# Kernel tuning notes

Hardware: AMD Instinct MI355X
Metric: run time of the kernel (lower is better)

The kernel has to match this reference:

```python
import jax, jax.numpy as jnp
import numpy as np

NEG_SLOPE = 0.2  # PyG GATConv default negative_slope


def gat_conv(x, W, b, a_src, a_dst, src, dst, N, H, C):
    """PyG-style GATConv (v1 attention), concat heads, self-loops already in (src,dst)."""
    h = (x @ W).reshape(N, H, C)                       # [N,H,C]
    al_src = jnp.sum(h * a_src, axis=-1)               # [N,H]
    al_dst = jnp.sum(h * a_dst, axis=-1)               # [N,H]
    e = jax.nn.leaky_relu(al_src[src] + al_dst[dst], NEG_SLOPE)  # [E,H]
    m = jax.ops.segment_max(e, dst, num_segments=N)    # segment softmax (stable)
    m = jnp.where(jnp.isfinite(m), m, 0.0)
    ex = jnp.exp(e - m[dst])
    denom = jax.ops.segment_sum(ex, dst, num_segments=N)
    alpha = ex / (denom[dst] + 1e-16)                  # [E,H]
    msg = h[src] * alpha[..., None]                    # [E,H,C]
    out = jax.ops.segment_sum(msg, dst, num_segments=N)  # [N,H,C]
    return out.reshape(N, H * C) + b


def setup_inputs() -> dict:
    key = jax.random.key(0)
    ks = jax.random.split(key, 16)
    N, E, IN, HID, HEADS, OUT, G = 50000, 600000, 128, 64, 4, 10, 64
    x = jax.random.normal(ks[0], (N, IN), dtype=jnp.float32)
    edge_index = jax.random.randint(ks[1], (2, E), 0, N, dtype=jnp.int32)
    batch = jnp.sort(jax.random.randint(ks[2], (N,), 0, G, dtype=jnp.int32))
    s = 0.1
    p = {
        'W1': jax.random.normal(ks[3], (IN, HEADS * HID)) * s,
        'b1': jnp.zeros((HEADS * HID,), jnp.float32),
        'asrc1': jax.random.normal(ks[4], (HEADS, HID)) * s,
        'adst1': jax.random.normal(ks[5], (HEADS, HID)) * s,
        'W2': jax.random.normal(ks[6], (HEADS * HID, HEADS * HID)) * s,
        'b2': jnp.zeros((HEADS * HID,), jnp.float32),
        'asrc2': jax.random.normal(ks[7], (HEADS, HID)) * s,
        'adst2': jax.random.normal(ks[8], (HEADS, HID)) * s,
        'W3': jax.random.normal(ks[9], (HEADS * HID, HID)) * s,
        'b3': jnp.zeros((HID,), jnp.float32),
        'asrc3': jax.random.normal(ks[10], (1, HID)) * s,
        'adst3': jax.random.normal(ks[11], (1, HID)) * s,
        'linW': jax.random.normal(ks[12], (HID, OUT)) * s,
        'linb': jnp.zeros((OUT,), jnp.float32),
    }
    return dict(x=x, edge_index=edge_index, batch=batch, **p)


def reference(x, edge_index, batch, W1, b1, asrc1, adst1, W2, b2, asrc2, adst2,
              W3, b3, asrc3, adst3, linW, linb):
    N = x.shape[0]
    G = 64  # number of graphs
    loops = jnp.arange(N, dtype=edge_index.dtype)
    src = jnp.concatenate([edge_index[0], loops])  # PyG adds self-loops by default
    dst = jnp.concatenate([edge_index[1], loops])
    # eval mode: dropout is identity
    h = jax.nn.elu(gat_conv(x, W1, b1, asrc1, adst1, src, dst, N, 4, 64))
    h = jax.nn.elu(gat_conv(h, W2, b2, asrc2, adst2, src, dst, N, 4, 64))
    h = jax.nn.elu(gat_conv(h, W3, b3, asrc3, adst3, src, dst, N, 1, 64))
    # global mean pool over graphs
    sums = jax.ops.segment_sum(h, batch, num_segments=G)            # [G,64]
    cnts = jax.ops.segment_sum(jnp.ones((N,), h.dtype), batch, num_segments=G)
    pooled = sums / jnp.maximum(cnts, 1.0)[:, None]
    return pooled @ linW + linb                                      # [G,10]
```

## Files before the change

kernel.cpp:

```cpp
#include <hip/hip_runtime.h>
#include <hip/hip_bf16.h>
#include <math.h>

#define NEG_SLOPE 0.2f

typedef short short8 __attribute__((ext_vector_type(8)));
typedef float f32x4 __attribute__((ext_vector_type(4)));
typedef unsigned int u32;
typedef unsigned short u16;

__device__ __forceinline__ float lrelu(float x){ return x > 0.f ? x : NEG_SLOPE * x; }
__device__ __forceinline__ float elu_f(float x){ return x > 0.f ? x : __expf(x) - 1.f; }
__device__ __forceinline__ float blo(u32 w){ return __uint_as_float(w << 16); }
__device__ __forceinline__ float bhi(u32 w){ return __uint_as_float(w & 0xffff0000u); }
__device__ __forceinline__ float bf2f(u16 u){ return __uint_as_float(((u32)u) << 16); }
__device__ __forceinline__ u16 f2bf(float f){
  __hip_bfloat16 h = __float2bfloat16(f);
  return *(u16*)&h;
}

__global__ void prep_kernel(const float* __restrict__ x, u16* __restrict__ xb, int n4,
                            const float* __restrict__ W1, u16* __restrict__ w1t,
                            const float* __restrict__ W2, u16* __restrict__ w2t,
                            const float* __restrict__ W3, u16* __restrict__ w3t,
                            int* __restrict__ cursor, int N){
  int i = blockIdx.x * 256 + threadIdx.x;
  if (i < n4){
    float4 v = ((const float4*)x)[i];
    ushort4 o;
    o.x = f2bf(v.x); o.y = f2bf(v.y); o.z = f2bf(v.z); o.w = f2bf(v.w);
    ((ushort4*)xb)[i] = o;
    return;
  }
  int t = i - n4;
  if (t < 128 * 256){
    int k = t >> 8, m = t & 255;
    w1t[m * 128 + k] = f2bf(W1[t]);
    return;
  }
  t -= 128 * 256;
  if (t < 256 * 256){
    int k = t >> 8, m = t & 255;
    w2t[m * 256 + k] = f2bf(W2[t]);
    return;
  }
  t -= 256 * 256;
  if (t < 256 * 64){
    int k = t >> 6, m = t & 63;
    w3t[m * 256 + k] = f2bf(W3[t]);
    return;
  }
  t -= 256 * 64;
  if (t < N) cursor[t] = 0;
}

__global__ void ell_kernel(const int* __restrict__ src, const int* __restrict__ dst,
                           int E, int* cursor, int* __restrict__ ell){
  int i = blockIdx.x * 256 + threadIdx.x;
  if (i < E){
    int s = src[i], d = dst[i];
    int pos = atomicAdd(&cursor[d], 1);
    if (pos < 64) ell[(size_t)d * 64 + pos] = s;
  }
}

template<int BN>
__global__ __launch_bounds__((BN == 256) ? 512 : 256) void gemm_mfma(
    const u16* __restrict__ A, const u16* __restrict__ Bt, u16* __restrict__ C,
    const float* __restrict__ asrc, const float* __restrict__ adst,
    float* __restrict__ als, float* __restrict__ ald, int N, int K, int M){
  constexpr int T  = (BN == 256) ? 512 : 256;
  constexpr int MI = (BN == 256) ? 4 : 2;
  constexpr int HH = BN / 64;
  constexpr int AQ = 1024 / T;
  constexpr int SB = BN * 8 / T;
  constexpr int LB = (BN == 256) ? 8 : 6;
  __shared__ short As[8][128][8];
  __shared__ short Bs[8][BN][8];
  const int tid = threadIdx.x;
  const int w = tid >> 6, lane = tid & 63;
  const int quad = lane >> 4, l16 = lane & 15;
  const int row0 = blockIdx.y * 128;
  const int wrow = (BN == 256) ? (w >> 2) * 64 : w * 32;
  const int wcol = (BN == 256) ? (w & 3) * 64 : 0;

  f32x4 acc[MI][4];
#pragma unroll
  for (int i = 0; i < MI; i++)
#pragma unroll
    for (int j = 0; j < 4; j++) acc[i][j] = (f32x4){0.f, 0.f, 0.f, 0.f};

  for (int k0 = 0; k0 < K; k0 += 64){
    __syncthreads();
#pragma unroll
    for (int q = 0; q < AQ; q++){
      int lb = q * T + w * 64;
      int li = lb + lane;
      int c = li >> 7, r = li & 127;
      int grow = min(row0 + r, N - 1);
      const u16* gp = A + (size_t)grow * K + k0 + c * 8;
      __builtin_amdgcn_global_load_lds((const __attribute__((address_space(1))) void*)gp,
                                       (__attribute__((address_space(3))) void*)((char*)&As[0][0][0] + (size_t)lb * 16),
                                       16, 0, 0);
    }
#pragma unroll
    for (int q = 0; q < SB; q++){
      int lb = q * T + w * 64;
      int li = lb + lane;
      int c = li >> LB, n = li & (BN - 1);
      const u16* gp = Bt + (size_t)n * K + k0 + c * 8;
      __builtin_amdgcn_global_load_lds((const __attribute__((address_space(1))) void*)gp,
                                       (__attribute__((address_space(3))) void*)((char*)&Bs[0][0][0] + (size_t)lb * 16),
                                       16, 0, 0);
    }
    __syncthreads();
#pragma unroll
    for (int ks = 0; ks < 2; ks++){
      short8 a[MI], b[4];
#pragma unroll
      for (int i = 0; i < MI; i++) a[i] = *(const short8*)&As[ks * 4 + quad][wrow + i * 16 + l16][0];
#pragma unroll
      for (int j = 0; j < 4; j++)  b[j] = *(const short8*)&Bs[ks * 4 + quad][wcol + j * 16 + l16][0];
#pragma unroll
      for (int i = 0; i < MI; i++)
#pragma unroll
        for (int j = 0; j < 4; j++)
          acc[i][j] = __builtin_amdgcn_mfma_f32_16x16x32_bf16(a[i], b[j], acc[i][j], 0, 0, 0);
    }
  }

  const int head = wcol >> 6;
  float avs[4], avd[4];
#pragma unroll
  for (int j = 0; j < 4; j++){
    int c = j * 16 + l16;
    avs[j] = asrc[head * 64 + c];
    avd[j] = adst[head * 64 + c];
  }

#pragma unroll
  for (int i = 0; i < MI; i++){
#pragma unroll
    for (int rr = 0; rr < 4; rr++){
      int row = row0 + wrow + i * 16 + quad * 4 + rr;
      float ps = acc[i][0][rr] * avs[0] + acc[i][1][rr] * avs[1]
               + acc[i][2][rr] * avs[2] + acc[i][3][rr] * avs[3];
      float pd = acc[i][0][rr] * avd[0] + acc[i][1][rr] * avd[1]
               + acc[i][2][rr] * avd[2] + acc[i][3][rr] * avd[3];
#pragma unroll
      for (int off = 8; off > 0; off >>= 1){
        ps += __shfl_xor(ps, off);
        pd += __shfl_xor(pd, off);
      }
      if (row < N){
#pragma unroll
        for (int j = 0; j < 4; j++)
          C[(size_t)row * M + wcol + j * 16 + l16] = f2bf(acc[i][j][rr]);
        if (l16 == 0){
          als[(size_t)row * HH + head] = ps;
          ald[(size_t)row * HH + head] = pd;
        }
      }
    }
  }
}

__global__ __launch_bounds__(256) void agg4_kernel(const u16* __restrict__ hb,
    const float* __restrict__ als, const float* __restrict__ ald,
    const int* __restrict__ degv, const int* __restrict__ ell,
    const float* __restrict__ bias, u16* __restrict__ out, int N){
  __shared__ float lex[4][256];
  __shared__ int lu[4][64];
  int wslot = threadIdx.x >> 6;
  int node = (blockIdx.x * 256 + threadIdx.x) >> 6;
  int lane = threadIdx.x & 63;
  if (node >= N) return;
  int deg = min(degv[node], 64);
  float4 t4 = *(const float4*)(ald + node * 4);
  const int hh = lane >> 4;

  bool v = lane < deg;
  int u = v ? ell[(size_t)node * 64 + lane] : 0;
  float4 s = *(const float4*)(als + (size_t)u * 4);
  float4 exv;
  exv.x = v ? __expf(lrelu(s.x + t4.x)) : 0.f;
  exv.y = v ? __expf(lrelu(s.y + t4.y)) : 0.f;
  exv.z = v ? __expf(lrelu(s.z + t4.z)) : 0.f;
  exv.w = v ? __expf(lrelu(s.w + t4.w)) : 0.f;
  *(float4*)&lex[wslot][lane * 4] = exv;
  lu[wslot][lane] = u;
  asm volatile("s_waitcnt lgkmcnt(0)" ::: "memory");

  const u16* hbl = hb + lane * 4;
  float4 ss = *(const float4*)(als + (size_t)node * 4);
  float es0 = __expf(lrelu(ss.x + t4.x));
  float es1 = __expf(lrelu(ss.y + t4.y));
  float es2 = __expf(lrelu(ss.z + t4.z));
  float es3 = __expf(lrelu(ss.w + t4.w));
  float exs = (hh == 0) ? es0 : (hh == 1) ? es1 : (hh == 2) ? es2 : es3;
  uint2 tself = *(const uint2*)(hbl + (size_t)node * 256);
  float denom = exs;
  float a0 = exs * blo(tself.x), a1 = exs * bhi(tself.x);
  float a2 = exs * blo(tself.y), a3 = exs * bhi(tself.y);

#pragma unroll 8
  for (int jj = 0; jj < deg; jj++){
    float ex = lex[wslot][jj * 4 + hh];
    int uu = lu[wslot][jj];
    uint2 t = *(const uint2*)(hbl + (size_t)uu * 256);
    denom += ex;
    a0 += ex * blo(t.x);
    a1 += ex * bhi(t.x);
    a2 += ex * blo(t.y);
    a3 += ex * bhi(t.y);
  }
  float inv = 1.f / (denom + 1e-16f);
  int ch = lane * 4;
  float o0 = elu_f(a0 * inv + bias[ch]);
  float o1 = elu_f(a1 * inv + bias[ch + 1]);
  float o2 = elu_f(a2 * inv + bias[ch + 2]);
  float o3 = elu_f(a3 * inv + bias[ch + 3]);
  uint2 o;
  o.x = (u32)f2bf(o0) | ((u32)f2bf(o1) << 16);
  o.y = (u32)f2bf(o2) | ((u32)f2bf(o3) << 16);
  ((uint2*)out)[(size_t)node * 64 + lane] = o;
}

__global__ __launch_bounds__(256) void agg1_kernel(const u16* __restrict__ hb,
    const float* __restrict__ als, const float* __restrict__ ald,
    const int* __restrict__ degv, const int* __restrict__ ell,
    const float* __restrict__ bias, u16* __restrict__ out, int N){
  __shared__ float lex[4][72];
  __shared__ int lu[4][72];
  int wslot = threadIdx.x >> 6;
  int node = (blockIdx.x * 256 + threadIdx.x) >> 6;
  int lane = threadIdx.x & 63;
  if (node >= N) return;
  int deg = min(degv[node], 64);
  float adv = ald[node];

  bool v = lane < deg;
  int u = v ? ell[(size_t)node * 64 + lane] : 0;
  lex[wslot][lane] = v ? __expf(lrelu(als[u] + adv)) : 0.f;
  lu[wslot][lane] = u;
  if (lane < 8){ lex[wslot][64 + lane] = 0.f; lu[wslot][64 + lane] = 0; }
  asm volatile("s_waitcnt lgkmcnt(0)" ::: "memory");

  int eo = lane >> 4;
  int chb = (lane & 15) * 4;
  float a0 = 0.f, a1 = 0.f, a2 = 0.f, a3 = 0.f, denom = 0.f;
  if (eo == 0){
    float exs = __expf(lrelu(als[node] + adv));
    uint2 t = *(const uint2*)(hb + (size_t)node * 64 + chb);
    denom = exs;
    a0 = exs * blo(t.x); a1 = exs * bhi(t.x);
    a2 = exs * blo(t.y); a3 = exs * bhi(t.y);
  }
#pragma unroll 4
  for (int j2 = 0; j2 < deg; j2 += 4){
    int jj = j2 + eo;
    float ex = lex[wslot][jj];
    int uu = lu[wslot][jj];
    uint2 t = *(const uint2*)(hb + (size_t)uu * 64 + chb);
    denom += ex;
    a0 += ex * blo(t.x);
    a1 += ex * bhi(t.x);
    a2 += ex * blo(t.y);
    a3 += ex * bhi(t.y);
  }
#pragma unroll
  for (int off = 16; off < 64; off <<= 1){
    denom += __shfl_xor(denom, off);
    a0 += __shfl_xor(a0, off); a1 += __shfl_xor(a1, off);
    a2 += __shfl_xor(a2, off); a3 += __shfl_xor(a3, off);
  }
  if (eo == 0){
    float inv = 1.f / (denom + 1e-16f);
    float o0 = elu_f(a0 * inv + bias[chb]);
    float o1 = elu_f(a1 * inv + bias[chb + 1]);
    float o2 = elu_f(a2 * inv + bias[chb + 2]);
    float o3 = elu_f(a3 * inv + bias[chb + 3]);
    uint2 o;
    o.x = (u32)f2bf(o0) | ((u32)f2bf(o1) << 16);
    o.y = (u32)f2bf(o2) | ((u32)f2bf(o3) << 16);
    *(uint2*)(out + (size_t)node * 64 + chb) = o;
  }
}

__global__ __launch_bounds__(256) void poolfinal_kernel(const u16* __restrict__ f,
    const int* __restrict__ batch, int N, const float* __restrict__ linW,
    const float* __restrict__ linb, float* __restrict__ out){
  const int g = blockIdx.x;
  const int w = threadIdx.x >> 6, lane = threadIdx.x & 63;
  int lo = 0, hi = N;
  while (lo < hi){ int m = (lo + hi) >> 1; if (batch[m] < g) lo = m + 1; else hi = m; }
  const int s0 = lo;
  lo = 0; hi = N;
  while (lo < hi){ int m = (lo + hi) >> 1; if (batch[m] < g + 1) lo = m + 1; else hi = m; }
  const int s1 = lo;

  float acc0 = 0.f, acc1 = 0.f, acc2 = 0.f, acc3 = 0.f;
  int n = s0 + w;
  for (; n + 12 < s1; n += 16){
    acc0 += bf2f(f[(size_t)n * 64 + lane]);
    acc1 += bf2f(f[(size_t)(n + 4) * 64 + lane]);
    acc2 += bf2f(f[(size_t)(n + 8) * 64 + lane]);
    acc3 += bf2f(f[(size_t)(n + 12) * 64 + lane]);
  }
  for (; n < s1; n += 4) acc0 += bf2f(f[(size_t)n * 64 + lane]);
  float acc = (acc0 + acc1) + (acc2 + acc3);

  __shared__ float red[4][64];
  red[w][lane] = acc;
  __syncthreads();
  if (threadIdx.x < 64){
    red[0][lane] = red[0][lane] + red[1][lane] + red[2][lane] + red[3][lane];
  }
  __syncthreads();
  if (threadIdx.x < 10){
    float c = fmaxf((float)(s1 - s0), 1.f);
    float a = 0.f;
#pragma unroll
    for (int k = 0; k < 64; k++) a += red[0][k] * linW[k * 10 + threadIdx.x];
    out[g * 10 + threadIdx.x] = a / c + linb[threadIdx.x];
  }
}

extern "C" void kernel_launch(void* const* d_in, const int* in_sizes, int n_in,
                              void* d_out, int out_size, void* d_ws, size_t ws_size,
                              hipStream_t stream) {
  const float* x     = (const float*)d_in[0];
  const int*   ei    = (const int*)  d_in[1];
  const int*   batch = (const int*)  d_in[2];
  const float* W1    = (const float*)d_in[3];
  const float* b1    = (const float*)d_in[4];
  const float* asrc1 = (const float*)d_in[5];
  const float* adst1 = (const float*)d_in[6];
  const float* W2    = (const float*)d_in[7];
  const float* b2    = (const float*)d_in[8];
  const float* asrc2 = (const float*)d_in[9];
  const float* adst2 = (const float*)d_in[10];
  const float* W3    = (const float*)d_in[11];
  const float* b3    = (const float*)d_in[12];
  const float* asrc3 = (const float*)d_in[13];
  const float* adst3 = (const float*)d_in[14];
  const float* linW  = (const float*)d_in[15];
  const float* linb  = (const float*)d_in[16];

  const int N = in_sizes[0] / 128;
  const int E = in_sizes[1] / 2;
  const int G = 64;
  const int* src = ei;
  const int* dst = ei + E;

  char* p = (char*)d_ws;
  auto carve = [&](size_t bytes) -> char* {
    char* r = p;
    p += (bytes + 255) & ~(size_t)255;
    return r;
  };
  u16*   xb       = (u16*)  carve((size_t)N * 128 * 2);
  u16*   w1t      = (u16*)  carve((size_t)256 * 128 * 2);
  u16*   w2t      = (u16*)  carve((size_t)256 * 256 * 2);
  u16*   w3t      = (u16*)  carve((size_t)64 * 256 * 2);
  u16*   hb       = (u16*)  carve((size_t)N * 256 * 2);
  u16*   featb    = (u16*)  carve((size_t)N * 256 * 2);
  u16*   out3     = (u16*)  carve((size_t)N * 64 * 2);
  float* als      = (float*)carve((size_t)N * 4 * 4);
  float* ald      = (float*)carve((size_t)N * 4 * 4);
  int*   cursor   = (int*)  carve((size_t)N * 4);
  int*   ell      = (int*)  carve((size_t)N * 64 * 4);

  const int n4 = N * 128 / 4;
  const int prep_items = n4 + 128 * 256 + 256 * 256 + 256 * 64 + N;

  prep_kernel<<<(prep_items + 255) / 256, 256, 0, stream>>>(x, xb, n4, W1, w1t, W2, w2t, W3, w3t,
                                                            cursor, N);

  ell_kernel<<<(E + 255) / 256, 256, 0, stream>>>(src, dst, E, cursor, ell);

  const int nby = (N + 127) / 128;
  const int wpn_grid = (N + 3) / 4;

  gemm_mfma<256><<<dim3(1, nby), 512, 0, stream>>>(xb, w1t, hb, asrc1, adst1, als, ald, N, 128, 256);
  agg4_kernel<<<wpn_grid, 256, 0, stream>>>(hb, als, ald, cursor, ell, b1, featb, N);

  gemm_mfma<256><<<dim3(1, nby), 512, 0, stream>>>(featb, w2t, hb, asrc2, adst2, als, ald, N, 256, 256);
  agg4_kernel<<<wpn_grid, 256, 0, stream>>>(hb, als, ald, cursor, ell, b2, featb, N);

  gemm_mfma<64><<<dim3(1, nby), 256, 0, stream>>>(featb, w3t, hb, asrc3, adst3, als, ald, N, 256, 64);
  agg1_kernel<<<wpn_grid, 256, 0, stream>>>(hb, als, ald, cursor, ell, b3, out3, N);

  poolfinal_kernel<<<G, 256, 0, stream>>>(out3, batch, N, linW, linb, (float*)d_out);
}
```

Measured before the change: 341.2 us.

## Fuse GAT aggregation into following layer's MFMA GEMM via LDS A-tile

Replaces the standalone 4-head aggregation kernels with a fused kernel. Each block aggregates 128 destination nodes directly into a swizzled LDS A tile, then runs the next layer's bf16 MFMA GEMM and attention-logit epilogue on that tile. This removes the write and re-read of the intermediate bf16 feature matrix and one launch per layer. Attention logits are ping-ponged between two buffers so the fused kernel never reads and writes the same array. The cost is far fewer blocks (one per 128 nodes) doing serial per-node gathers, which may expose gather latency and lower occupancy because of the large LDS footprint.

Measured after the change: 476.9 us. +39.8%, slower.

```diff
diff --git a/kernel.cpp b/kernel.cpp
--- a/kernel.cpp
+++ b/kernel.cpp
@@ -165,65 +165,163 @@
   }
 }
 
-__global__ __launch_bounds__(256) void agg4_kernel(const u16* __restrict__ hb,
-    const float* __restrict__ als, const float* __restrict__ ald,
+template<int BN>
+__global__ __launch_bounds__((BN == 256) ? 512 : 256) void fused_agg_gemm(
+    const u16* __restrict__ Gsrc,
+    const float* __restrict__ als_in, const float* __restrict__ ald_in,
     const int* __restrict__ degv, const int* __restrict__ ell,
-    const float* __restrict__ bias, u16* __restrict__ out, int N){
-  __shared__ float lex[4][256];
-  __shared__ int lu[4][64];
-  int wslot = threadIdx.x >> 6;
-  int node = (blockIdx.x * 256 + threadIdx.x) >> 6;
-  int lane = threadIdx.x & 63;
-  if (node >= N) return;
-  int deg = min(degv[node], 64);
-  float4 t4 = *(const float4*)(ald + node * 4);
+    const float* __restrict__ bias_in,
+    const u16* __restrict__ Bt, u16* __restrict__ C,
+    const float* __restrict__ asrc, const float* __restrict__ adst,
+    float* __restrict__ als_out, float* __restrict__ ald_out, int N){
+  constexpr int K   = 256;
+  constexpr int T   = (BN == 256) ? 512 : 256;
+  constexpr int W   = T / 64;
+  constexpr int NPW = 128 / W;
+  constexpr int MI  = (BN == 256) ? 4 : 2;
+  constexpr int HH  = BN / 64;
+  constexpr int SB  = BN * 8 / T;
+  constexpr int LB  = (BN == 256) ? 8 : 6;
+  __shared__ short As[128][32][8];
+  __shared__ short Bs[8][BN][8];
+  __shared__ float lexs[W][256];
+  __shared__ int   lus[W][64];
+  const int tid = threadIdx.x;
+  const int w = tid >> 6, lane = tid & 63;
+  const int quad = lane >> 4, l16 = lane & 15;
+  const int row0 = blockIdx.x * 128;
+  const int wrow = (BN == 256) ? (w >> 2) * 64 : w * 32;
+  const int wcol = (BN == 256) ? (w & 3) * 64 : 0;
   const int hh = lane >> 4;
 
-  bool v = lane < deg;
-  int u = v ? ell[(size_t)node * 64 + lane] : 0;
-  float4 s = *(const float4*)(als + (size_t)u * 4);
-  float4 exv;
-  exv.x = v ? __expf(lrelu(s.x + t4.x)) : 0.f;
-  exv.y = v ? __expf(lrelu(s.y + t4.y)) : 0.f;
-  exv.z = v ? __expf(lrelu(s.z + t4.z)) : 0.f;
-  exv.w = v ? __expf(lrelu(s.w + t4.w)) : 0.f;
-  *(float4*)&lex[wslot][lane * 4] = exv;
-  lu[wslot][lane] = u;
-  asm volatile("s_waitcnt lgkmcnt(0)" ::: "memory");
-
-  const u16* hbl = hb + lane * 4;
-  float4 ss = *(const float4*)(als + (size_t)node * 4);
-  float es0 = __expf(lrelu(ss.x + t4.x));
-  float es1 = __expf(lrelu(ss.y + t4.y));
-  float es2 = __expf(lrelu(ss.z + t4.z));
-  float es3 = __expf(lrelu(ss.w + t4.w));
-  float exs = (hh == 0) ? es0 : (hh == 1) ? es1 : (hh == 2) ? es2 : es3;
-  uint2 tself = *(const uint2*)(hbl + (size_t)node * 256);
-  float denom = exs;
-  float a0 = exs * blo(tself.x), a1 = exs * bhi(tself.x);
-  float a2 = exs * blo(tself.y), a3 = exs * bhi(tself.y);
-
+  for (int nn = 0; nn < NPW; nn++){
+    int r = w * NPW + nn;
+    int node = row0 + r;
+    float o0 = 0.f, o1 = 0.f, o2 = 0.f, o3 = 0.f;
+    if (node < N){
+      int deg = min(degv[node], 64);
+      float4 t4 = *(const float4*)(ald_in + (size_t)node * 4);
+      bool v = lane < deg;
+      int u = v ? ell[(size_t)node * 64 + lane] : 0;
+      float4 s = *(const float4*)(als_in + (size_t)u * 4);
+      float4 exv;
+      exv.x = v ? __expf(lrelu(s.x + t4.x)) : 0.f;
+      exv.y = v ? __expf(lrelu(s.y + t4.y)) : 0.f;
+      exv.z = v ? __expf(lrelu(s.z + t4.z)) : 0.f;
+      exv.w = v ? __expf(lrelu(s.w + t4.w)) : 0.f;
+      *(float4*)&lexs[w][lane * 4] = exv;
+      lus[w][lane] = u;
+      asm volatile("s_waitcnt lgkmcnt(0)" ::: "memory");
+
+      const u16* gl = Gsrc + lane * 4;
+      float4 ss = *(const float4*)(als_in + (size_t)node * 4);
+      float es0 = __expf(lrelu(ss.x + t4.x));
+      float es1 = __expf(lrelu(ss.y + t4.y));
+      float es2 = __expf(lrelu(ss.z + t4.z));
+      float es3 = __expf(lrelu(ss.w + t4.w));
+      float exs = (hh == 0) ? es0 : (hh == 1) ? es1 : (hh == 2) ? es2 : es3;
+      uint2 tself = *(const uint2*)(gl + (size_t)node * 256);
+      float denom = exs;
+      float a0 = exs * blo(tself.x), a1 = exs * bhi(tself.x);
+      float a2 = exs * blo(tself.y), a3 = exs * bhi(tself.y);
 #pragma unroll 8
-  for (int jj = 0; jj < deg; jj++){
-    float ex = lex[wslot][jj * 4 + hh];
-    int uu = lu[wslot][jj];
-    uint2 t = *(const uint2*)(hbl + (size_t)uu * 256);
-    denom += ex;
-    a0 += ex * blo(t.x);
-    a1 += ex * bhi(t.x);
-    a2 += ex * blo(t.y);
-    a3 += ex * bhi(t.y);
-  }
-  float inv = 1.f / (denom + 1e-16f);
-  int ch = lane * 4;
-  float o0 = elu_f(a0 * inv + bias[ch]);
-  float o1 = elu_f(a1 * inv + bias[ch + 1]);
-  float o2 = elu_f(a2 * inv + bias[ch + 2]);
-  float o3 = elu_f(a3 * inv + bias[ch + 3]);
-  uint2 o;
-  o.x = (u32)f2bf(o0) | ((u32)f2bf(o1) << 16);
-  o.y = (u32)f2bf(o2) | ((u32)f2bf(o3) << 16);
-  ((uint2*)out)[(size_t)node * 64 + lane] = o;
+      for (int jj = 0; jj < deg; jj++){
+        float ex = lexs[w][jj * 4 + hh];
+        int uu = lus[w][jj];
+        uint2 t = *(const uint2*)(gl + (size_t)uu * 256);
+        denom += ex;
+        a0 += ex * blo(t.x);
+        a1 += ex * bhi(t.x);
+        a2 += ex * blo(t.y);
+        a3 += ex * bhi(t.y);
+      }
+      float inv = 1.f / (denom + 1e-16f);
+      int ch = lane * 4;
+      o0 = elu_f(a0 * inv + bias_in[ch]);
+      o1 = elu_f(a1 * inv + bias_in[ch + 1]);
+      o2 = elu_f(a2 * inv + bias_in[ch + 2]);
+      o3 = elu_f(a3 * inv + bias_in[ch + 3]);
+    }
+    uint2 pk;
+    pk.x = (u32)f2bf(o0) | ((u32)f2bf(o1) << 16);
+    pk.y = (u32)f2bf(o2) | ((u32)f2bf(o3) << 16);
+    int bo = (r * 512 + lane * 8) ^ ((r & 7) << 4);
+    *(uint2*)((char*)&As[0][0][0] + bo) = pk;
+  }
+
+  f32x4 acc[MI][4];
+#pragma unroll
+  for (int i = 0; i < MI; i++)
+#pragma unroll
+    for (int j = 0; j < 4; j++) acc[i][j] = (f32x4){0.f, 0.f, 0.f, 0.f};
+
+  for (int t = 0; t < 4; t++){
+    __syncthreads();
+#pragma unroll
+    for (int q = 0; q < SB; q++){
+      int lb = q * T + w * 64;
+      int li = lb + lane;
+      int c = li >> LB, n = li & (BN - 1);
+      const u16* gp = Bt + (size_t)n * K + t * 64 + c * 8;
+      __builtin_amdgcn_global_load_lds((const __attribute__((address_space(1))) void*)gp,
+                                       (__attribute__((address_space(3))) void*)((char*)&Bs[0][0][0] + (size_t)lb * 16),
+                                       16, 0, 0);
+    }
+    __syncthreads();
+#pragma unroll
+    for (int ks = 0; ks < 2; ks++){
+      int kg = t * 8 + ks * 4 + quad;
+      short8 a[MI], b[4];
+#pragma unroll
+      for (int i = 0; i < MI; i++){
+        int row = wrow + i * 16 + l16;
+        int bo = (row * 512 + kg * 16) ^ ((row & 7) << 4);
+        a[i] = *(const short8*)((const char*)&As[0][0][0] + bo);
+      }
+#pragma unroll
+      for (int j = 0; j < 4; j++) b[j] = *(const short8*)&Bs[ks * 4 + quad][wcol + j * 16 + l16][0];
+#pragma unroll
+      for (int i = 0; i < MI; i++)
+#pragma unroll
+        for (int j = 0; j < 4; j++)
+          acc[i][j] = __builtin_amdgcn_mfma_f32_16x16x32_bf16(a[i], b[j], acc[i][j], 0, 0, 0);
+    }
+  }
+
+  const int head = wcol >> 6;
+  float avs[4], avd[4];
+#pragma unroll
+  for (int j = 0; j < 4; j++){
+    int c = j * 16 + l16;
+    avs[j] = asrc[head * 64 + c];
+    avd[j] = adst[head * 64 + c];
+  }
+
+#pragma unroll
+  for (int i = 0; i < MI; i++){
+#pragma unroll
+    for (int rr = 0; rr < 4; rr++){
+      int row = row0 + wrow + i * 16 + quad * 4 + rr;
+      float ps = acc[i][0][rr] * avs[0] + acc[i][1][rr] * avs[1]
+               + acc[i][2][rr] * avs[2] + acc[i][3][rr] * avs[3];
+      float pd = acc[i][0][rr] * avd[0] + acc[i][1][rr] * avd[1]
+               + acc[i][2][rr] * avd[2] + acc[i][3][rr] * avd[3];
+#pragma unroll
+      for (int off = 8; off > 0; off >>= 1){
+        ps += __shfl_xor(ps, off);
+        pd += __shfl_xor(pd, off);
+      }
+      if (row < N){
+#pragma unroll
+        for (int j = 0; j < 4; j++)
+          C[(size_t)row * BN + wcol + j * 16 + l16] = f2bf(acc[i][j][rr]);
+        if (l16 == 0){
+          als_out[(size_t)row * HH + head] = ps;
+          ald_out[(size_t)row * HH + head] = pd;
+        }
+      }
+    }
+  }
 }
 
 __global__ __launch_bounds__(256) void agg1_kernel(const u16* __restrict__ hb,
@@ -366,8 +464,10 @@
   u16*   hb       = (u16*)  carve((size_t)N * 256 * 2);
   u16*   featb    = (u16*)  carve((size_t)N * 256 * 2);
   u16*   out3     = (u16*)  carve((size_t)N * 64 * 2);
-  float* als      = (float*)carve((size_t)N * 4 * 4);
-  float* ald      = (float*)carve((size_t)N * 4 * 4);
+  float* alsA     = (float*)carve((size_t)N * 4 * 4);
+  float* aldA     = (float*)carve((size_t)N * 4 * 4);
+  float* alsB     = (float*)carve((size_t)N * 4 * 4);
+  float* aldB     = (float*)carve((size_t)N * 4 * 4);
   int*   cursor   = (int*)  carve((size_t)N * 4);
   int*   ell      = (int*)  carve((size_t)N * 64 * 4);
 
@@ -382,14 +482,15 @@
   const int nby = (N + 127) / 128;
   const int wpn_grid = (N + 3) / 4;
 
-  gemm_mfma<256><<<dim3(1, nby), 512, 0, stream>>>(xb, w1t, hb, asrc1, adst1, als, ald, N, 128, 256);
-  agg4_kernel<<<wpn_grid, 256, 0, stream>>>(hb, als, ald, cursor, ell, b1, featb, N);
-
-  gemm_mfma<256><<<dim3(1, nby), 512, 0, stream>>>(featb, w2t, hb, asrc2, adst2, als, ald, N, 256, 256);
-  agg4_kernel<<<wpn_grid, 256, 0, stream>>>(hb, als, ald, cursor, ell, b2, featb, N);
-
-  gemm_mfma<64><<<dim3(1, nby), 256, 0, stream>>>(featb, w3t, hb, asrc3, adst3, als, ald, N, 256, 64);
-  agg1_kernel<<<wpn_grid, 256, 0, stream>>>(hb, als, ald, cursor, ell, b3, out3, N);
+  gemm_mfma<256><<<dim3(1, nby), 512, 0, stream>>>(xb, w1t, hb, asrc1, adst1, alsA, aldA, N, 128, 256);
+
+  fused_agg_gemm<256><<<nby, 512, 0, stream>>>(hb, alsA, aldA, cursor, ell, b1,
+                                               w2t, featb, asrc2, adst2, alsB, aldB, N);
+
+  fused_agg_gemm<64><<<nby, 256, 0, stream>>>(featb, alsB, aldB, cursor, ell, b2,
+                                              w3t, hb, asrc3, adst3, alsA, aldA, N);
+
+  agg1_kernel<<<wpn_grid, 256, 0, stream>>>(hb, alsA, aldA, cursor, ell, b3, out3, N);
 
   poolfinal_kernel<<<G, 256, 0, stream>>>(out3, batch, N, linW, linb, (float*)d_out);
 }
```
